# Kernel optimization log

Measured on AMD Instinct MI355X. Metric: run time of the kernel, lower is better.

## Reference

```python
import jax, jax.numpy as jnp
import numpy as np

V, D, N, DK, DV, H, DFF = 32000, 512, 6, 64, 64, 8, 2048
B, S = 8, 512
EPS = 1e-5


def _pe(seq_len, d_model):
    pos = np.arange(seq_len)[:, None].astype(np.float32)
    i = np.arange(0, d_model, 2).astype(np.float32)
    ang = pos / np.power(10000.0, i / d_model)
    pe = np.zeros((seq_len, d_model), dtype=np.float32)
    pe[:, 0::2] = np.sin(ang)
    pe[:, 1::2] = np.cos(ang)
    return jnp.asarray(pe)


def _ln(x, g, b):
    m = jnp.mean(x, axis=-1, keepdims=True)
    v = jnp.mean(jnp.square(x - m), axis=-1, keepdims=True)
    return (x - m) * jax.lax.rsqrt(v + EPS) * g + b


def _mha(xq, xkv, Wq, Wk, Wv, bq, bk, bv, mask):
    # Wq/Wk: [H,D,DK], Wv: [H,D,DV]; mask: [B,Sq,Skv] additive
    q = jnp.einsum('bsd,hdk->bhsk', xq, Wq) + bq[None, :, None, :]
    k = jnp.einsum('bsd,hdk->bhsk', xkv, Wk) + bk[None, :, None, :]
    v = jnp.einsum('bsd,hdk->bhsk', xkv, Wv) + bv[None, :, None, :]
    scores = jnp.einsum('bhqk,bhsk->bhqs', q, k) / jnp.sqrt(jnp.float32(DK))
    scores = scores + mask[:, None, :, :]
    attn = jax.nn.softmax(scores, axis=-1)
    out = jnp.einsum('bhqs,bhsv->bhqv', attn, v)  # [B,H,Sq,DV]
    return out.transpose(0, 2, 1, 3).reshape(xq.shape[0], xq.shape[1], H * DV)


def setup_inputs() -> dict:
    key = jax.random.key(0)
    ks = jax.random.split(key, 24)
    sc = 0.02
    inp = {
        'decoder_input': jax.random.randint(ks[0], (B, S), 0, V),
        'encoder_output': jax.random.normal(ks[1], (B, S, D), dtype=jnp.float32),
        'self_mask': jnp.where(jnp.tril(jnp.ones((S, S), dtype=bool)), 0.0, -1e9)[None].repeat(B, 0).astype(jnp.float32),
        'cross_mask': jnp.zeros((B, S, S), dtype=jnp.float32),
        'emb': jax.random.normal(ks[2], (V, D), dtype=jnp.float32),
        'Wq_s': jax.random.normal(ks[3], (N, H, D, DK)) * sc,
        'Wk_s': jax.random.normal(ks[4], (N, H, D, DK)) * sc,
        'Wv_s': jax.random.normal(ks[5], (N, H, D, DV)) * sc,
        'bq_s': jnp.zeros((N, H, DK)), 'bk_s': jnp.zeros((N, H, DK)), 'bv_s': jnp.zeros((N, H, DV)),
        'Wq_c': jax.random.normal(ks[6], (N, H, D, DK)) * sc,
        'Wk_c': jax.random.normal(ks[7], (N, H, D, DK)) * sc,
        'Wv_c': jax.random.normal(ks[8], (N, H, D, DV)) * sc,
        'bq_c': jnp.zeros((N, H, DK)), 'bk_c': jnp.zeros((N, H, DK)), 'bv_c': jnp.zeros((N, H, DV)),
        'W1': jax.random.normal(ks[9], (N, D, DFF)) * sc,
        'b1': jnp.zeros((N, DFF)),
        'W2': jax.random.normal(ks[10], (N, DFF, D)) * sc,
        'b2': jnp.zeros((N, D)),
        'ln1_g': jnp.ones((N, D)), 'ln1_b': jnp.zeros((N, D)),
        'ln2_g': jnp.ones((N, D)), 'ln2_b': jnp.zeros((N, D)),
    }
    return inp


def reference(decoder_input, encoder_output, self_mask, cross_mask, emb,
              Wq_s, Wk_s, Wv_s, bq_s, bk_s, bv_s,
              Wq_c, Wk_c, Wv_c, bq_c, bk_c, bv_c,
              W1, b1, W2, b2, ln1_g, ln1_b, ln2_g, ln2_b):
    x = emb[decoder_input] + _pe(decoder_input.shape[1], D)[None]
    for l in range(N):
        sa = _mha(x, x, Wq_s[l], Wk_s[l], Wv_s[l], bq_s[l], bk_s[l], bv_s[l], self_mask)
        x = _ln(x + sa, ln1_g[l], ln1_b[l])
        ca = _mha(x, encoder_output, Wq_c[l], Wk_c[l], Wv_c[l], bq_c[l], bk_c[l], bv_c[l], cross_mask)
        x = _ln(x + ca, ln2_g[l], ln2_b[l])
        ff = jax.nn.relu(jnp.einsum('bsd,df->bsf', x, W1[l]) + b1[l])
        ff = jnp.einsum('bsf,fd->bsd', ff, W2[l]) + b2[l]
        # source reuses layer_norm2 for the third norm (layer_norm3 is dead)
        x = _ln(x + ff, ln2_g[l], ln2_b[l])
    return x
```

## Files before the change

### kernel.cpp

```cpp
#include <hip/hip_runtime.h>
#include <hip/hip_bf16.h>
#include <math.h>

#define BB 8
#define SS 512
#define DDIM 512
#define HH 8
#define DFFV 2048
#define NLAYER 6
#define EPSV 1e-5f
#define WQS 0.180336880f

typedef __attribute__((ext_vector_type(8))) short bf16x8;
typedef __attribute__((ext_vector_type(4))) float f32x4;

static __device__ __forceinline__ ushort f2bf(float f) {
  union { float f; unsigned u; } uf; uf.f = f;
  unsigned u = uf.u;
  unsigned r = (u + 0x7fffu + ((u >> 16) & 1u)) >> 16;
  return (ushort)r;
}
static __device__ __forceinline__ float bf2f(ushort h) {
  union { unsigned u; float f; } x;
  x.u = ((unsigned)h) << 16;
  return x.f;
}

static __device__ __forceinline__ void gload_lds16(const void* g, void* l) {
  __builtin_amdgcn_global_load_lds(
      (const __attribute__((address_space(1))) void*)g,
      (__attribute__((address_space(3))) void*)l, 16, 0, 0);
}

__global__ __launch_bounds__(256) void embed_pe_kernel(
    const int* __restrict__ idx, const float* __restrict__ emb,
    ushort* __restrict__ xb) {
  int t = blockIdx.x * blockDim.x + threadIdx.x;
  if (t >= BB * SS * DDIM) return;
  int d = t & (DDIM - 1);
  int bs = t >> 9;
  int s = bs & (SS - 1);
  int tok = idx[bs];
  int i2 = d & ~1;
  float ang = (float)s * powf(10000.0f, -((float)i2) / (float)DDIM);
  float pe = (d & 1) ? cosf(ang) : sinf(ang);
  float v = emb[tok * DDIM + d] + pe;
  xb[t] = f2bf(v);
}

__global__ __launch_bounds__(256) void cast_bf16_kernel(
    const float* __restrict__ in, ushort* __restrict__ out, int n4) {
  int t = blockIdx.x * blockDim.x + threadIdx.x;
  if (t >= n4) return;
  float4 v = reinterpret_cast<const float4*>(in)[t];
  ushort4 o;
  o.x = f2bf(v.x); o.y = f2bf(v.y); o.z = f2bf(v.z); o.w = f2bf(v.w);
  reinterpret_cast<ushort4*>(out)[t] = o;
}

__global__ __launch_bounds__(256) void wtrans_kernel(
    const float* __restrict__ in, ushort* __restrict__ out, int R, int C,
    int lgH, size_t zl, float scale) {
  __shared__ float t[32][33];
  int z = blockIdx.z;
  int l = z >> lgH, hh = z & ((1 << lgH) - 1);
  const float* ip = in + (size_t)z * R * C;
  ushort* op = out + (size_t)l * zl + (size_t)hh * R * C;
  int j = threadIdx.x & 31, i0 = threadIdx.x >> 5;
  int r0 = blockIdx.y * 32, c0 = blockIdx.x * 32;
#pragma unroll
  for (int p = 0; p < 4; p++) {
    int r = r0 + i0 + p * 8;
    t[i0 + p * 8][j] = ip[(size_t)r * C + c0 + j];
  }
  __syncthreads();
#pragma unroll
  for (int p = 0; p < 4; p++) {
    int cc = c0 + i0 + p * 8;
    op[(size_t)cc * R + r0 + j] = f2bf(t[j][i0 + p * 8] * scale);
  }
}

__global__ __launch_bounds__(256) void pack_bias_kernel(
    const float* __restrict__ bq, const float* __restrict__ bk,
    const float* __restrict__ bv, const float* __restrict__ bkc,
    const float* __restrict__ bvc, const float* __restrict__ bqc,
    float* __restrict__ qkvb, float* __restrict__ ckvb,
    float* __restrict__ cqb) {
  int t = blockIdx.x * 256 + threadIdx.x;
  if (t < NLAYER * 1536) {
    int l = t / 1536, n = t % 1536;
    float v = n < 512 ? bq[l * 512 + n] * WQS
                      : (n < 1024 ? bk[l * 512 + n - 512] : bv[l * 512 + n - 1024]);
    qkvb[t] = v;
  }
  if (t < NLAYER * 1024) {
    int l = t / 1024, n = t % 1024;
    ckvb[t] = n < 512 ? bkc[l * 512 + n] : bvc[l * 512 + n - 512];
  }
  if (t < NLAYER * 512) cqb[t] = bqc[t] * WQS;
}

template <int BM, int BN, int RELU, int OUTBF, int NTV, int LGP, int SPLITK,
          int SWZ>
__global__ __launch_bounds__(256) void gemm_mfma(
    const ushort* __restrict__ A, const ushort* __restrict__ Bw,
    const float* __restrict__ bias, float* __restrict__ Cf,
    ushort* __restrict__ Cb, ushort* __restrict__ vt, int M, int N, int K) {
  constexpr int WM = BM / 64;
  constexpr int WN = 4 / WM;
  constexpr int W = BN / WN;
  constexpr int AF = 4;
  constexpr int BF = W / 16;
  constexpr int GA = BM * 8;
  constexpr int GPT = (BM + BN) * 8 / 256;
  __shared__ __align__(16) ushort lds_s[2][(BM + BN) * 64];
  int bn, bm;
  if (SWZ) {
    int nwg = gridDim.x * gridDim.y;
    int wg = blockIdx.y * gridDim.x + blockIdx.x;
    int cpx = nwg >> 3;
    int swz = (wg & 7) * cpx + (wg >> 3);
    bn = (swz % gridDim.x) * BN;
    bm = (swz / gridDim.x) * BM;
  } else {
    bn = blockIdx.x * BN;
    bm = blockIdx.y * BM;
  }
  int kz = (SPLITK > 1) ? blockIdx.z : 0;
  int Keff = K / SPLITK;
  int kbase = kz * Keff;
  int tid = threadIdx.x, lane = tid & 63, w = tid >> 6;
  int wm = w / WN, wn = w % WN;
  int c = lane & 15, g16 = lane >> 4;
  f32x4 acc[AF][BF] = {};

  auto STAGE = [&](int k0, int bufi) {
#pragma unroll
    for (int i = 0; i < GPT; i++) {
      int gidx = i * 256 + tid;
      int gbase = (i * 4 + w) * 64;
      const ushort* src;
      if (gidx < GA) {
        int row = gidx >> 3, dg = gidx & 7;
        src = A + (size_t)(bm + row) * K + kbase + k0 + ((dg ^ (row & 7)) << 3);
      } else {
        int bidx = gidx - GA;
        int row = bidx >> 3, dg = bidx & 7;
        src = Bw + (size_t)(bn + row) * K + kbase + k0 + ((dg ^ (row & 7)) << 3);
      }
      gload_lds16(src, (void*)((char*)(&lds_s[bufi][0]) + gbase * 16));
    }
  };

  int nk = Keff >> 6;
  STAGE(0, 0);
  for (int kt = 0; kt < nk; kt++) {
    int cur = kt & 1;
    if (kt + 1 < nk) {
      STAGE((kt + 1) << 6, cur ^ 1);
      asm volatile("s_waitcnt vmcnt(%0)" ::"n"(GPT) : "memory");
    } else {
      asm volatile("s_waitcnt vmcnt(0)" ::: "memory");
    }
    __builtin_amdgcn_s_barrier();
    __builtin_amdgcn_sched_barrier(0);
    const ushort* Alds = &lds_s[cur][0];
    const ushort* Blds = &lds_s[cur][BM * 64];
#pragma unroll
    for (int ks = 0; ks < 2; ks++) {
      int g = ks * 4 + g16;
      bf16x8 a[AF], b[BF];
#pragma unroll
      for (int i = 0; i < AF; i++) {
        int R = wm * 64 + i * 16 + c;
        a[i] = *(const bf16x8*)(Alds + R * 64 + ((g ^ (R & 7)) << 3));
      }
#pragma unroll
      for (int j = 0; j < BF; j++) {
        int Rb = wn * W + j * 16 + c;
        b[j] = *(const bf16x8*)(Blds + Rb * 64 + ((g ^ (Rb & 7)) << 3));
      }
#pragma unroll
      for (int i = 0; i < AF; i++)
#pragma unroll
        for (int j = 0; j < BF; j++)
          acc[i][j] = __builtin_amdgcn_mfma_f32_16x16x32_bf16(a[i], b[j],
                                                              acc[i][j], 0, 0, 0);
    }
    __builtin_amdgcn_sched_barrier(0);
    __builtin_amdgcn_s_barrier();
  }
  int rb = g16 * 4;
#pragma unroll
  for (int j = 0; j < BF; j++) {
    int col = bn + wn * W + j * 16 + c;
    float bv = (SPLITK > 1 && kz != 0) ? 0.0f : bias[col];
    int cc = LGP ? (col & ((1 << LGP) - 1)) : col;
    int lp = LGP ? (col >> LGP) : 0;
    if (NTV > 0 && cc >= NTV) {
      int hh = (cc - NTV) >> 6, dv = col & 63;
      ushort* vtl = vt + (size_t)lp * 2097152;
#pragma unroll
      for (int i = 0; i < AF; i++) {
        int row = bm + wm * 64 + i * 16 + rb;
        int b_ = row >> 9, s_ = row & 511;
        ushort4 o4;
        o4.x = f2bf(acc[i][j][0] + bv);
        o4.y = f2bf(acc[i][j][1] + bv);
        o4.z = f2bf(acc[i][j][2] + bv);
        o4.w = f2bf(acc[i][j][3] + bv);
        *reinterpret_cast<ushort4*>(
            vtl + ((size_t)(b_ * 8 + hh) * 64 + dv) * 512 + s_) = o4;
      }
    } else {
#pragma unroll
      for (int i = 0; i < AF; i++) {
#pragma unroll
        for (int qq = 0; qq < 4; qq++) {
          int row = bm + wm * 64 + i * 16 + rb + qq;
          float v = acc[i][j][qq] + bv;
          if (RELU) v = fmaxf(v, 0.0f);
          if (OUTBF)
            Cb[(size_t)row * N + col] = f2bf(v);
          else
            Cf[(size_t)kz * M * N + (size_t)row * N + col] = v;
        }
      }
    }
  }
}

template <int MASKED, int NW>
__global__ __launch_bounds__(NW * 64) void attn_mfma(
    const ushort* __restrict__ q, int qstr, const ushort* __restrict__ k,
    int kstr, const ushort* __restrict__ vt, ushort* __restrict__ out) {
  __shared__ __align__(16) char lds[32768 + NW * 2048];
  int h = blockIdx.y, b = blockIdx.z;
  int qc = blockIdx.x;
  if (MASKED && (b & 4)) qc = gridDim.x - 1 - qc;
  int q0 = qc * (NW * 16);
  int tid = threadIdx.x, lane = tid & 63, w = tid >> 6;
  int c = lane & 15, g16 = lane >> 4, rb = g16 * 4;

  bf16x8 qa[2];
#pragma unroll
  for (int ks = 0; ks < 2; ks++)
    qa[ks] = *(const bf16x8*)(q + (size_t)(b * SS + q0 + 16 * w + c) * qstr +
                              h * 64 + ks * 32 + g16 * 8);
  f32x4 o[4] = {};
  float mq = -1e30f, lq = 0.f;

  int nt = MASKED ? (q0 >> 6) + 1 : 8;
  int pbase = 32768 + w * 2048;

  constexpr int GPTK = 512 / (NW * 64);
  bf16x8 rk[GPTK], rv[GPTK];
  const ushort* vbase = vt + ((size_t)(b * 8 + h) * 64) * 512;
  auto LOADT = [&](int kv0) {
#pragma unroll
    for (int i = 0; i < GPTK; i++) {
      int idx = tid + i * (NW * 64);
      int row = idx >> 3, gw = idx & 7;
      rk[i] = *(const bf16x8*)(k + (size_t)(b * SS + kv0 + row) * kstr +
                               h * 64 + gw * 8);
      rv[i] = *(const bf16x8*)(vbase + (size_t)row * 512 + kv0 + gw * 8);
    }
  };
  auto WRT = [&](int bufi) {
    char* p = lds + bufi * 16384;
#pragma unroll
    for (int i = 0; i < GPTK; i++) {
      int idx = tid + i * (NW * 64);
      int row = idx >> 3, gw = idx & 7;
      *(bf16x8*)(p + row * 128 + ((gw ^ (row & 7)) << 4)) = rk[i];
      *(bf16x8*)(p + 8192 + row * 128 + ((gw ^ (row & 7)) << 4)) = rv[i];
    }
  };
  LOADT(0);
  WRT(0);
  for (int t = 0; t < nt; t++) {
    if (t + 1 < nt) LOADT((t + 1) * 64);
    __syncthreads();
    char* kb_ = lds + (t & 1) * 16384;
    char* vb_ = kb_ + 8192;
    f32x4 sp[4] = {};
    __builtin_amdgcn_s_setprio(1);
#pragma unroll
    for (int ks = 0; ks < 2; ks++) {
      int g = ks * 4 + g16;
#pragma unroll
      for (int f = 0; f < 4; f++) {
        int row = f * 16 + c;
        bf16x8 k8 = *(bf16x8*)(kb_ + row * 128 + ((g ^ (row & 7)) << 4));
        sp[f] = __builtin_amdgcn_mfma_f32_16x16x32_bf16(k8, qa[ks], sp[f], 0, 0, 0);
      }
    }
    __builtin_amdgcn_s_setprio(0);
    if (MASKED && t == nt - 1) {
      int ql = 16 * w + c;
#pragma unroll
      for (int f = 0; f < 4; f++)
#pragma unroll
        for (int j = 0; j < 4; j++)
          sp[f][j] += (f * 16 + rb + j) <= ql ? 0.0f : -1e9f;
    }
    float tmax = -1e30f;
#pragma unroll
    for (int f = 0; f < 4; f++)
#pragma unroll
      for (int j = 0; j < 4; j++) tmax = fmaxf(tmax, sp[f][j]);
    tmax = fmaxf(tmax, __shfl_xor(tmax, 16));
    tmax = fmaxf(tmax, __shfl_xor(tmax, 32));
    if (!__all(tmax <= mq + 4.0f)) {
      float mn = fmaxf(mq, tmax);
      float scq = exp2f(mq - mn);
      mq = mn;
      lq *= scq;
      int sb = lane & 48;
#pragma unroll
      for (int j = 0; j < 4; j++) {
        float scj = __shfl(scq, sb | (rb + j));
        o[0][j] *= scj; o[1][j] *= scj; o[2][j] *= scj; o[3][j] *= scj;
      }
    }
    float psum = 0.f;
#pragma unroll
    for (int f = 0; f < 4; f++)
#pragma unroll
      for (int j = 0; j < 4; j++) {
        float pv = exp2f(sp[f][j] - mq);
        sp[f][j] = pv;
        psum += pv;
      }
    psum += __shfl_xor(psum, 16);
    psum += __shfl_xor(psum, 32);
    lq += psum;
#pragma unroll
    for (int f = 0; f < 4; f++) {
      int kv0 = f * 16 + rb;
      ushort4 pk;
      pk.x = f2bf(sp[f][0]); pk.y = f2bf(sp[f][1]);
      pk.z = f2bf(sp[f][2]); pk.w = f2bf(sp[f][3]);
      int gg = kv0 >> 3, off = (kv0 & 7) * 2;
      *(ushort4*)(lds + pbase + c * 128 + ((gg ^ (c & 7)) << 4) + off) = pk;
    }
    __builtin_amdgcn_s_setprio(1);
#pragma unroll
    for (int ks2 = 0; ks2 < 2; ks2++) {
      int g = ks2 * 4 + g16;
      bf16x8 pa = *(bf16x8*)(lds + pbase + c * 128 + ((g ^ (c & 7)) << 4));
#pragma unroll
      for (int f = 0; f < 4; f++) {
        int row = f * 16 + c;
        bf16x8 v8 = *(bf16x8*)(vb_ + row * 128 + ((g ^ (row & 7)) << 4));
        o[f] = __builtin_amdgcn_mfma_f32_16x16x32_bf16(pa, v8, o[f], 0, 0, 0);
      }
    }
    __builtin_amdgcn_s_setprio(0);
    if (t + 1 < nt) WRT((t + 1) & 1);
  }
  float invq = 1.0f / lq;
  int sb = lane & 48;
#pragma unroll
  for (int j = 0; j < 4; j++) {
    float invj = __shfl(invq, sb | (rb + j));
    size_t rowo = (size_t)(b * SS + q0 + 16 * w + rb + j) * 512 + h * 64;
#pragma unroll
    for (int f = 0; f < 4; f++)
      out[rowo + f * 16 + c] = f2bf(o[f][j] * invj);
  }
}

template <int Y2>
__global__ __launch_bounds__(256) void add_ln_kernel(
    ushort* __restrict__ xb, const ushort* __restrict__ yb,
    const float* __restrict__ y0, const float* __restrict__ y1,
    const float* __restrict__ g, const float* __restrict__ bta,
    float* __restrict__ xf) {
  int row = blockIdx.x * 4 + (threadIdx.x >> 6);
  int lane = threadIdx.x & 63;
  int base = row * DDIM + lane * 8;
  bf16x8 xv = *reinterpret_cast<const bf16x8*>(xb + base);
  float v[8];
  if (Y2) {
    float4 a0 = *reinterpret_cast<const float4*>(y0 + base);
    float4 a1 = *reinterpret_cast<const float4*>(y0 + base + 4);
    float4 c0 = *reinterpret_cast<const float4*>(y1 + base);
    float4 c1 = *reinterpret_cast<const float4*>(y1 + base + 4);
    v[0] = bf2f((ushort)xv[0]) + a0.x + c0.x;
    v[1] = bf2f((ushort)xv[1]) + a0.y + c0.y;
    v[2] = bf2f((ushort)xv[2]) + a0.z + c0.z;
    v[3] = bf2f((ushort)xv[3]) + a0.w + c0.w;
    v[4] = bf2f((ushort)xv[4]) + a1.x + c1.x;
    v[5] = bf2f((ushort)xv[5]) + a1.y + c1.y;
    v[6] = bf2f((ushort)xv[6]) + a1.z + c1.z;
    v[7] = bf2f((ushort)xv[7]) + a1.w + c1.w;
  } else {
    bf16x8 yv = *reinterpret_cast<const bf16x8*>(yb + base);
#pragma unroll
    for (int i = 0; i < 8; i++)
      v[i] = bf2f((ushort)xv[i]) + bf2f((ushort)yv[i]);
  }
  float s = 0.f;
#pragma unroll
  for (int i = 0; i < 8; i++) s += v[i];
#pragma unroll
  for (int off = 32; off > 0; off >>= 1) s += __shfl_xor(s, off);
  float mean = s * (1.0f / DDIM);
  float t2 = 0.f;
#pragma unroll
  for (int i = 0; i < 8; i++) {
    v[i] -= mean;
    t2 += v[i] * v[i];
  }
#pragma unroll
  for (int off = 32; off > 0; off >>= 1) t2 += __shfl_xor(t2, off);
  float rs = rsqrtf(t2 * (1.0f / DDIM) + EPSV);
  int cidx = lane * 8;
  float4 g0 = *reinterpret_cast<const float4*>(g + cidx);
  float4 g1 = *reinterpret_cast<const float4*>(g + cidx + 4);
  float4 b0 = *reinterpret_cast<const float4*>(bta + cidx);
  float4 b1 = *reinterpret_cast<const float4*>(bta + cidx + 4);
  float o[8];
  o[0] = v[0] * rs * g0.x + b0.x; o[1] = v[1] * rs * g0.y + b0.y;
  o[2] = v[2] * rs * g0.z + b0.z; o[3] = v[3] * rs * g0.w + b0.w;
  o[4] = v[4] * rs * g1.x + b1.x; o[5] = v[5] * rs * g1.y + b1.y;
  o[6] = v[6] * rs * g1.z + b1.z; o[7] = v[7] * rs * g1.w + b1.w;
  bf16x8 ob;
#pragma unroll
  for (int i = 0; i < 8; i++) ob[i] = (short)f2bf(o[i]);
  *reinterpret_cast<bf16x8*>(xb + base) = ob;
  if (xf) {
    float4 w0 = {o[0], o[1], o[2], o[3]}, w1 = {o[4], o[5], o[6], o[7]};
    *reinterpret_cast<float4*>(xf + base) = w0;
    *reinterpret_cast<float4*>(xf + base + 4) = w1;
  }
}

extern "C" void kernel_launch(void* const* d_in, const int* in_sizes, int n_in,
                              void* d_out, int out_size, void* d_ws,
                              size_t ws_size, hipStream_t stream) {
  const int* dec = (const int*)d_in[0];
  const float* enc = (const float*)d_in[1];
  const float* emb = (const float*)d_in[4];
  const float* Wq_s = (const float*)d_in[5];
  const float* Wk_s = (const float*)d_in[6];
  const float* Wv_s = (const float*)d_in[7];
  const float* bq_s = (const float*)d_in[8];
  const float* bk_s = (const float*)d_in[9];
  const float* bv_s = (const float*)d_in[10];
  const float* Wq_c = (const float*)d_in[11];
  const float* Wk_c = (const float*)d_in[12];
  const float* Wv_c = (const float*)d_in[13];
  const float* bq_c = (const float*)d_in[14];
  const float* bk_c = (const float*)d_in[15];
  const float* bv_c = (const float*)d_in[16];
  const float* W1 = (const float*)d_in[17];
  const float* b1 = (const float*)d_in[18];
  const float* W2 = (const float*)d_in[19];
  const float* b2 = (const float*)d_in[20];
  const float* ln1_g = (const float*)d_in[21];
  const float* ln1_b = (const float*)d_in[22];
  const float* ln2_g = (const float*)d_in[23];
  const float* ln2_b = (const float*)d_in[24];

  char* ws = (char*)d_ws;
  ushort* wqkv = (ushort*)(ws + 0);
  ushort* wqc = (ushort*)(ws + 9437184ull);
  ushort* wckv = (ushort*)(ws + 12582912ull);
  ushort* w1t = (ushort*)(ws + 18874368ull);
  ushort* w2t = (ushort*)(ws + 31457280ull);
  ushort* encb = (ushort*)(ws + 44040192ull);
  ushort* xb = (ushort*)(ws + 48234496ull);
  ushort* tmpb = (ushort*)(ws + 52428800ull);
  float* tmpf = (float*)(ws + 56623104ull);
  ushort* qkvbuf = (ushort*)(ws + 73400320ull);
  ushort* cq = (ushort*)(ws + 73400320ull);
  ushort* ff1b = (ushort*)(ws + 73400320ull);
  ushort* vt = (ushort*)(ws + 85983232ull);
  float* qkvbias = (float*)(ws + 90177536ull);
  float* ckvbias = (float*)(ws + 90214400ull);
  ushort* ckvbuf = (ushort*)(ws + 90238976ull);
  ushort* vtc = (ushort*)(ws + 140570624ull);
  float* cqbias = (float*)(ws + 165736448ull);

  const int M = BB * SS;
  dim3 g256(256);

  embed_pe_kernel<<<dim3((M * DDIM + 255) / 256), g256, 0, stream>>>(dec, emb,
                                                                     xb);
  cast_bf16_kernel<<<dim3(M * DDIM / 4 / 256), g256, 0, stream>>>(
      enc, encb, M * DDIM / 4);
  pack_bias_kernel<<<dim3(36), g256, 0, stream>>>(bq_s, bk_s, bv_s, bk_c, bv_c,
                                                  bq_c, qkvbias, ckvbias,
                                                  cqbias);

  wtrans_kernel<<<dim3(2, 16, 48), g256, 0, stream>>>(Wq_s, wqkv, 512, 64, 3,
                                                      786432ull, WQS);
  wtrans_kernel<<<dim3(2, 16, 48), g256, 0, stream>>>(Wk_s, wqkv + 262144, 512,
                                                      64, 3, 786432ull, 1.0f);
  wtrans_kernel<<<dim3(2, 16, 48), g256, 0, stream>>>(Wv_s, wqkv + 524288, 512,
                                                      64, 3, 786432ull, 1.0f);
  wtrans_kernel<<<dim3(2, 16, 48), g256, 0, stream>>>(Wq_c, wqc, 512, 64, 3,
                                                      262144ull, WQS);
  wtrans_kernel<<<dim3(2, 16, 48), g256, 0, stream>>>(Wk_c, wckv, 512, 64, 3,
                                                      524288ull, 1.0f);
  wtrans_kernel<<<dim3(2, 16, 48), g256, 0, stream>>>(Wv_c, wckv + 262144, 512,
                                                      64, 3, 524288ull, 1.0f);
  wtrans_kernel<<<dim3(64, 16, 6), g256, 0, stream>>>(W1, w1t, 512, 2048, 0,
                                                      1048576ull, 1.0f);
  wtrans_kernel<<<dim3(16, 64, 6), g256, 0, stream>>>(W2, w2t, 2048, 512, 0,
                                                      1048576ull, 1.0f);

  gemm_mfma<128, 128, 0, 1, 512, 10, 1, 0><<<dim3(48, 32), g256, 0, stream>>>(
      encb, wckv, ckvbias, nullptr, ckvbuf, vtc, M, 6144, 512);

  for (int l = 0; l < NLAYER; l++) {
    gemm_mfma<64, 128, 0, 1, 1024, 0, 1, 1><<<dim3(12, 64), g256, 0, stream>>>(
        xb, wqkv + (size_t)l * 786432, qkvbias + l * 1536, nullptr, qkvbuf, vt,
        M, 1536, 512);
    attn_mfma<1, 4><<<dim3(8, 8, 8), g256, 0, stream>>>(
        qkvbuf, 1536, qkvbuf + 512, 1536, vt, tmpb);
    add_ln_kernel<0><<<dim3(M / 4), g256, 0, stream>>>(
        xb, tmpb, nullptr, nullptr, ln1_g + l * 512, ln1_b + l * 512, nullptr);
    gemm_mfma<64, 128, 0, 1, 0, 0, 1, 1><<<dim3(4, 64), g256, 0, stream>>>(
        xb, wqc + (size_t)l * 262144, cqbias + l * 512, nullptr, cq, nullptr,
        M, 512, 512);
    attn_mfma<0, 8><<<dim3(4, 8, 8), dim3(512), 0, stream>>>(
        cq, 512, ckvbuf + l * 1024, 6144, vtc + (size_t)l * 2097152, tmpb);
    add_ln_kernel<0><<<dim3(M / 4), g256, 0, stream>>>(
        xb, tmpb, nullptr, nullptr, ln2_g + l * 512, ln2_b + l * 512, nullptr);
    gemm_mfma<64, 128, 1, 1, 0, 0, 1, 1><<<dim3(16, 64), g256, 0, stream>>>(
        xb, w1t + (size_t)l * 1048576, b1 + l * DFFV, nullptr, ff1b, nullptr,
        M, DFFV, 512);
    gemm_mfma<64, 128, 0, 0, 0, 0, 2, 1><<<dim3(4, 64, 2), g256, 0, stream>>>(
        ff1b, w2t + (size_t)l * 1048576, b2 + l * 512, tmpf, nullptr, nullptr,
        M, 512, DFFV);
    add_ln_kernel<1><<<dim3(M / 4), g256, 0, stream>>>(
        xb, nullptr, tmpf, tmpf + (size_t)M * 512, ln2_g + l * 512,
        ln2_b + l * 512, (l == NLAYER - 1) ? (float*)d_out : nullptr);
  }
}
```

Measured before the change: 638.5 us.

## Fuse prep kernels and stage GEMM epilogue through LDS for vectorized stores

Merges the embedding+PE, encoder cast, and bias packing kernels into one launch, and folds the six attention weight transposes into a single kernel, cutting launch count. The GEMM epilogue for bf16 outputs (both row-major and the transposed V layout) now writes tiles to LDS first and then emits 16-byte coalesced global stores instead of scattered 2- or 8-byte stores. This adds a __syncthreads and reuses the operand LDS buffer after the main loop.

```diff
diff --git a/kernel.cpp b/kernel.cpp
--- a/kernel.cpp
+++ b/kernel.cpp
@@ -32,30 +32,51 @@
       (__attribute__((address_space(3))) void*)l, 16, 0, 0);
 }
 
-__global__ __launch_bounds__(256) void embed_pe_kernel(
+__global__ __launch_bounds__(256) void prep_kernel(
     const int* __restrict__ idx, const float* __restrict__ emb,
-    ushort* __restrict__ xb) {
-  int t = blockIdx.x * blockDim.x + threadIdx.x;
-  if (t >= BB * SS * DDIM) return;
-  int d = t & (DDIM - 1);
-  int bs = t >> 9;
-  int s = bs & (SS - 1);
-  int tok = idx[bs];
-  int i2 = d & ~1;
-  float ang = (float)s * powf(10000.0f, -((float)i2) / (float)DDIM);
-  float pe = (d & 1) ? cosf(ang) : sinf(ang);
-  float v = emb[tok * DDIM + d] + pe;
-  xb[t] = f2bf(v);
-}
-
-__global__ __launch_bounds__(256) void cast_bf16_kernel(
-    const float* __restrict__ in, ushort* __restrict__ out, int n4) {
-  int t = blockIdx.x * blockDim.x + threadIdx.x;
-  if (t >= n4) return;
-  float4 v = reinterpret_cast<const float4*>(in)[t];
-  ushort4 o;
-  o.x = f2bf(v.x); o.y = f2bf(v.y); o.z = f2bf(v.z); o.w = f2bf(v.w);
-  reinterpret_cast<ushort4*>(out)[t] = o;
+    const float* __restrict__ enc, const float* __restrict__ bq,
+    const float* __restrict__ bk, const float* __restrict__ bv,
+    const float* __restrict__ bkc, const float* __restrict__ bvc,
+    const float* __restrict__ bqc, ushort* __restrict__ xb,
+    ushort* __restrict__ encb, float* __restrict__ qkvb,
+    float* __restrict__ ckvb, float* __restrict__ cqb) {
+  int gid = blockIdx.x * 256 + threadIdx.x;
+  {
+    int t0 = gid * 4;
+    int bs = t0 >> 9;
+    int s = bs & (SS - 1);
+    int tok = idx[bs];
+    ushort4 o;
+    float vv[4];
+#pragma unroll
+    for (int e = 0; e < 4; e++) {
+      int d = (t0 + e) & (DDIM - 1);
+      int i2 = d & ~1;
+      float ang = (float)s * powf(10000.0f, -((float)i2) / (float)DDIM);
+      float pe = (d & 1) ? cosf(ang) : sinf(ang);
+      vv[e] = emb[(size_t)tok * DDIM + d] + pe;
+    }
+    o.x = f2bf(vv[0]); o.y = f2bf(vv[1]); o.z = f2bf(vv[2]); o.w = f2bf(vv[3]);
+    *reinterpret_cast<ushort4*>(xb + t0) = o;
+  }
+  {
+    float4 v = reinterpret_cast<const float4*>(enc)[gid];
+    ushort4 o;
+    o.x = f2bf(v.x); o.y = f2bf(v.y); o.z = f2bf(v.z); o.w = f2bf(v.w);
+    reinterpret_cast<ushort4*>(encb)[gid] = o;
+  }
+  int t = gid;
+  if (t < NLAYER * 1536) {
+    int l = t / 1536, n = t % 1536;
+    float v = n < 512 ? bq[l * 512 + n] * WQS
+                      : (n < 1024 ? bk[l * 512 + n - 512] : bv[l * 512 + n - 1024]);
+    qkvb[t] = v;
+  }
+  if (t < NLAYER * 1024) {
+    int l = t / 1024, n = t % 1024;
+    ckvb[t] = n < 512 ? bkc[l * 512 + n] : bvc[l * 512 + n - 512];
+  }
+  if (t < NLAYER * 512) cqb[t] = bqc[t] * WQS;
 }
 
 __global__ __launch_bounds__(256) void wtrans_kernel(
@@ -81,24 +102,40 @@
   }
 }
 
-__global__ __launch_bounds__(256) void pack_bias_kernel(
-    const float* __restrict__ bq, const float* __restrict__ bk,
-    const float* __restrict__ bv, const float* __restrict__ bkc,
-    const float* __restrict__ bvc, const float* __restrict__ bqc,
-    float* __restrict__ qkvb, float* __restrict__ ckvb,
-    float* __restrict__ cqb) {
-  int t = blockIdx.x * 256 + threadIdx.x;
-  if (t < NLAYER * 1536) {
-    int l = t / 1536, n = t % 1536;
-    float v = n < 512 ? bq[l * 512 + n] * WQS
-                      : (n < 1024 ? bk[l * 512 + n - 512] : bv[l * 512 + n - 1024]);
-    qkvb[t] = v;
-  }
-  if (t < NLAYER * 1024) {
-    int l = t / 1024, n = t % 1024;
-    ckvb[t] = n < 512 ? bkc[l * 512 + n] : bvc[l * 512 + n - 512];
-  }
-  if (t < NLAYER * 512) cqb[t] = bqc[t] * WQS;
+__global__ __launch_bounds__(256) void wtrans6_kernel(
+    const float* __restrict__ qs, const float* __restrict__ ks,
+    const float* __restrict__ vs, const float* __restrict__ qc,
+    const float* __restrict__ kc, const float* __restrict__ vc,
+    ushort* __restrict__ wqkv, ushort* __restrict__ wqc,
+    ushort* __restrict__ wckv) {
+  __shared__ float t[32][33];
+  int z = blockIdx.z;
+  int job = z / 48, zz = z % 48;
+  const float* in; ushort* out; size_t zl; float scale;
+  switch (job) {
+    case 0: in = qs; out = wqkv;           zl = 786432; scale = WQS; break;
+    case 1: in = ks; out = wqkv + 262144;  zl = 786432; scale = 1.f; break;
+    case 2: in = vs; out = wqkv + 524288;  zl = 786432; scale = 1.f; break;
+    case 3: in = qc; out = wqc;            zl = 262144; scale = WQS; break;
+    case 4: in = kc; out = wckv;           zl = 524288; scale = 1.f; break;
+    default: in = vc; out = wckv + 262144; zl = 524288; scale = 1.f; break;
+  }
+  int l = zz >> 3, hh = zz & 7;
+  const float* ip = in + (size_t)zz * 512 * 64;
+  ushort* op = out + (size_t)l * zl + (size_t)hh * 512 * 64;
+  int j = threadIdx.x & 31, i0 = threadIdx.x >> 5;
+  int r0 = blockIdx.y * 32, c0 = blockIdx.x * 32;
+#pragma unroll
+  for (int p = 0; p < 4; p++) {
+    int r = r0 + i0 + p * 8;
+    t[i0 + p * 8][j] = ip[(size_t)r * 64 + c0 + j];
+  }
+  __syncthreads();
+#pragma unroll
+  for (int p = 0; p < 4; p++) {
+    int cc = c0 + i0 + p * 8;
+    op[(size_t)cc * 512 + r0 + j] = f2bf(t[j][i0 + p * 8] * scale);
+  }
 }
 
 template <int BM, int BN, int RELU, int OUTBF, int NTV, int LGP, int SPLITK,
@@ -192,39 +229,81 @@
     __builtin_amdgcn_s_barrier();
   }
   int rb = g16 * 4;
-#pragma unroll
-  for (int j = 0; j < BF; j++) {
-    int col = bn + wn * W + j * 16 + c;
-    float bv = (SPLITK > 1 && kz != 0) ? 0.0f : bias[col];
-    int cc = LGP ? (col & ((1 << LGP) - 1)) : col;
-    int lp = LGP ? (col >> LGP) : 0;
-    if (NTV > 0 && cc >= NTV) {
-      int hh = (cc - NTV) >> 6, dv = col & 63;
-      ushort* vtl = vt + (size_t)lp * 2097152;
+  int cc0 = LGP ? (bn & ((1 << LGP) - 1)) : bn;
+  bool isV = (NTV > 0) && (cc0 >= NTV);
+  if (isV) {
+    constexpr int CST = BM + 8;
+    ushort* tl = (ushort*)lds_s;
+#pragma unroll
+    for (int j = 0; j < BF; j++) {
+      int colL = wn * W + j * 16 + c;
+      float bv = bias[bn + colL];
 #pragma unroll
       for (int i = 0; i < AF; i++) {
-        int row = bm + wm * 64 + i * 16 + rb;
-        int b_ = row >> 9, s_ = row & 511;
+        int rowL0 = wm * 64 + i * 16 + rb;
         ushort4 o4;
         o4.x = f2bf(acc[i][j][0] + bv);
         o4.y = f2bf(acc[i][j][1] + bv);
         o4.z = f2bf(acc[i][j][2] + bv);
         o4.w = f2bf(acc[i][j][3] + bv);
-        *reinterpret_cast<ushort4*>(
-            vtl + ((size_t)(b_ * 8 + hh) * 64 + dv) * 512 + s_) = o4;
-      }
-    } else {
+        *reinterpret_cast<ushort4*>(tl + colL * CST + rowL0) = o4;
+      }
+    }
+    __syncthreads();
+    int colL = tid >> 1, half = tid & 1;
+    int col = bn + colL;
+    int cc = LGP ? (col & ((1 << LGP) - 1)) : col;
+    int lp = LGP ? (col >> LGP) : 0;
+    int hh = (cc - NTV) >> 6, dv = col & 63;
+    ushort* vtl = vt + (size_t)lp * 2097152;
+    int b_ = bm >> 9;
+    int s0 = (bm & 511) + half * (BM / 2);
+    ushort* dst = vtl + ((size_t)(b_ * 8 + hh) * 64 + dv) * 512 + s0;
+    const ushort* srcl = tl + colL * CST + half * (BM / 2);
+#pragma unroll
+    for (int u = 0; u < BM / 16; u++)
+      *reinterpret_cast<bf16x8*>(dst + u * 8) =
+          *reinterpret_cast<const bf16x8*>(srcl + u * 8);
+  } else if (OUTBF) {
+    constexpr int RST = BN + 8;
+    ushort* tl = (ushort*)lds_s;
+#pragma unroll
+    for (int j = 0; j < BF; j++) {
+      int colL = wn * W + j * 16 + c;
+      float bv = bias[bn + colL];
+#pragma unroll
+      for (int i = 0; i < AF; i++) {
+        int rowL0 = wm * 64 + i * 16 + rb;
+#pragma unroll
+        for (int qq = 0; qq < 4; qq++) {
+          float v = acc[i][j][qq] + bv;
+          if (RELU) v = fmaxf(v, 0.0f);
+          tl[(rowL0 + qq) * RST + colL] = f2bf(v);
+        }
+      }
+    }
+    __syncthreads();
+    constexpr int TPR = 256 / BM;
+    constexpr int CPT = BN / TPR;
+    int rowL = tid / TPR, qp = tid % TPR;
+    int c0i = qp * CPT;
+    ushort* dst = Cb + (size_t)(bm + rowL) * N + bn + c0i;
+    const ushort* srcl = tl + rowL * RST + c0i;
+#pragma unroll
+    for (int u = 0; u < CPT / 8; u++)
+      *reinterpret_cast<bf16x8*>(dst + u * 8) =
+          *reinterpret_cast<const bf16x8*>(srcl + u * 8);
+  } else {
+#pragma unroll
+    for (int j = 0; j < BF; j++) {
+      int col = bn + wn * W + j * 16 + c;
+      float bv = (SPLITK > 1 && kz != 0) ? 0.0f : bias[col];
 #pragma unroll
       for (int i = 0; i < AF; i++) {
 #pragma unroll
         for (int qq = 0; qq < 4; qq++) {
           int row = bm + wm * 64 + i * 16 + rb + qq;
-          float v = acc[i][j][qq] + bv;
-          if (RELU) v = fmaxf(v, 0.0f);
-          if (OUTBF)
-            Cb[(size_t)row * N + col] = f2bf(v);
-          else
-            Cf[(size_t)kz * M * N + (size_t)row * N + col] = v;
+          Cf[(size_t)kz * M * N + (size_t)row * N + col] = acc[i][j][qq] + bv;
         }
       }
     }
@@ -488,26 +567,11 @@
   const int M = BB * SS;
   dim3 g256(256);
 
-  embed_pe_kernel<<<dim3((M * DDIM + 255) / 256), g256, 0, stream>>>(dec, emb,
-                                                                     xb);
-  cast_bf16_kernel<<<dim3(M * DDIM / 4 / 256), g256, 0, stream>>>(
-      enc, encb, M * DDIM / 4);
-  pack_bias_kernel<<<dim3(36), g256, 0, stream>>>(bq_s, bk_s, bv_s, bk_c, bv_c,
-                                                  bq_c, qkvbias, ckvbias,
-                                                  cqbias);
-
-  wtrans_kernel<<<dim3(2, 16, 48), g256, 0, stream>>>(Wq_s, wqkv, 512, 64, 3,
-                                                      786432ull, WQS);
-  wtrans_kernel<<<dim3(2, 16, 48), g256, 0, stream>>>(Wk_s, wqkv + 262144, 512,
-                                                      64, 3, 786432ull, 1.0f);
-  wtrans_kernel<<<dim3(2, 16, 48), g256, 0, stream>>>(Wv_s, wqkv + 524288, 512,
-                                                      64, 3, 786432ull, 1.0f);
-  wtrans_kernel<<<dim3(2, 16, 48), g256, 0, stream>>>(Wq_c, wqc, 512, 64, 3,
-                                                      262144ull, WQS);
-  wtrans_kernel<<<dim3(2, 16, 48), g256, 0, stream>>>(Wk_c, wckv, 512, 64, 3,
-                                                      524288ull, 1.0f);
-  wtrans_kernel<<<dim3(2, 16, 48), g256, 0, stream>>>(Wv_c, wckv + 262144, 512,
-                                                      64, 3, 524288ull, 1.0f);
+  prep_kernel<<<dim3(2048), g256, 0, stream>>>(dec, emb, enc, bq_s, bk_s, bv_s,
+                                               bk_c, bv_c, bq_c, xb, encb,
+                                               qkvbias, ckvbias, cqbias);
+  wtrans6_kernel<<<dim3(2, 16, 288), g256, 0, stream>>>(
+      Wq_s, Wk_s, Wv_s, Wq_c, Wk_c, Wv_c, wqkv, wqc, wckv);
   wtrans_kernel<<<dim3(64, 16, 6), g256, 0, stream>>>(W1, w1t, 512, 2048, 0,
                                                       1048576ull, 1.0f);
   wtrans_kernel<<<dim3(16, 64, 6), g256, 0, stream>>>(W2, w2t, 2048, 512, 0,
```

Result: slower. 675.3 us (+5.8%).
